# Kernel optimization log

Hardware: AMD Instinct MI355X
Metric: run time of the kernel (lower is better)

Reference implementation:

```python
import jax, jax.numpy as jnp
import numpy as np
import itertools

B, RES, RES_, STRIDE = 256, 14, 7, 2
N, N_ = RES * RES, RES_ * RES_
IN_DIM, OUT_DIM = 384, 512
H, KD, AR = 12, 32, 2
D = AR * KD            # 64, per-head value dim
DH = D * H             # 768
NH_KD = KD * H         # 384
KV_H = DH + NH_KD      # 1152
EPS = 1e-5


def _bias_idxs():
    # Replicates the relative-offset indexing from __init__.
    points = list(itertools.product(range(RES), range(RES)))
    points_ = list(itertools.product(range(RES_), range(RES_)))
    offsets, idxs = {}, []
    for p1 in points_:
        for p2 in points:
            off = (abs(p1[0] * STRIDE - p2[0]), abs(p1[1] * STRIDE - p2[1]))
            if off not in offsets:
                offsets[off] = len(offsets)
            idxs.append(offsets[off])
    return np.array(idxs, dtype=np.int32).reshape(N_, N), len(offsets)


def linear_bn(x, w, gamma, beta, mean, var):
    # Linear (no bias) followed by BatchNorm1d in inference form (fused affine).
    s = gamma / jnp.sqrt(var + EPS)
    return jnp.matmul(x, w.T) * s + (beta - mean * s)


def setup_inputs() -> dict:
    key = jax.random.key(0)
    ks = jax.random.split(key, 12)
    idxs_np, n_off = _bias_idxs()

    def bn_params(k, dim):
        k1, k2, k3, k4 = jax.random.split(k, 4)
        return (jax.random.normal(k1, (dim,)) * 0.1 + 1.0,   # gamma
                jax.random.normal(k2, (dim,)) * 0.1,          # beta
                jax.random.normal(k3, (dim,)) * 0.1,          # running_mean
                jax.random.uniform(k4, (dim,), minval=0.5, maxval=1.5))  # running_var

    kv_g, kv_b, kv_m, kv_v = bn_params(ks[1], KV_H)
    q_g, q_b, q_m, q_v = bn_params(ks[3], NH_KD)
    pr_g, pr_b, pr_m, pr_v = bn_params(ks[5], OUT_DIM)

    return {
        "x": jax.random.normal(ks[0], (B, N, IN_DIM), dtype=jnp.float32),
        "kv_w": jax.random.normal(ks[6], (KV_H, IN_DIM), dtype=jnp.float32) * (IN_DIM ** -0.5),
        "kv_g": kv_g, "kv_b": kv_b, "kv_m": kv_m, "kv_v": kv_v,
        "q_w": jax.random.normal(ks[7], (NH_KD, IN_DIM), dtype=jnp.float32) * (IN_DIM ** -0.5),
        "q_g": q_g, "q_b": q_b, "q_m": q_m, "q_v": q_v,
        "proj_w": jax.random.normal(ks[8], (OUT_DIM, DH), dtype=jnp.float32) * (DH ** -0.5),
        "proj_g": pr_g, "proj_b": pr_b, "proj_m": pr_m, "proj_v": pr_v,
        "attention_biases": jax.random.normal(ks[9], (H, n_off), dtype=jnp.float32) * 0.02,
        "bias_idxs": jnp.asarray(idxs_np),
    }


def reference(x, kv_w, kv_g, kv_b, kv_m, kv_v,
              q_w, q_g, q_b, q_m, q_v,
              proj_w, proj_g, proj_b, proj_m, proj_v,
              attention_biases, bias_idxs):
    Bsz = x.shape[0]
    scale = KD ** -0.5
    # kv projection: [B, N, H, KD+D] -> split into k, v
    kv = linear_bn(x, kv_w, kv_g, kv_b, kv_m, kv_v).reshape(Bsz, N, H, KD + D)
    k, v = kv[..., :KD], kv[..., KD:]
    # strided subsample of queries: [B, 14, 14, C] -> [B, 49, C]
    xs = x.reshape(Bsz, RES, RES, IN_DIM)[:, ::STRIDE, ::STRIDE].reshape(Bsz, N_, IN_DIM)
    q = linear_bn(xs, q_w, q_g, q_b, q_m, q_v).reshape(Bsz, N_, H, KD)
    # attention with gathered relative-position bias: bias [H, N_, N]
    bias = attention_biases[:, bias_idxs]
    attn = jnp.einsum('bqhd,bkhd->bhqk', q, k) * scale + bias
    attn = jax.nn.softmax(attn, axis=-1)
    out = jnp.einsum('bhqk,bkhd->bqhd', attn, v).reshape(Bsz, N_, DH)
    out = jax.nn.hard_swish(out)
    return linear_bn(out, proj_w, proj_g, proj_b, proj_m, proj_v)
```

## Files before the change

kernel.cpp:

```cpp
#include <hip/hip_runtime.h>
#include <hip/hip_bf16.h>
#include <math.h>

typedef unsigned short U16;
typedef unsigned int U32;
typedef __attribute__((ext_vector_type(8))) short bf8;
typedef __attribute__((ext_vector_type(4))) float f4;
typedef __attribute__((ext_vector_type(4))) unsigned short u16x4;

#define AS1 __attribute__((address_space(1)))
#define AS3 __attribute__((address_space(3)))

#define BSZ   256
#define NTOK  196
#define NQ    49
#define INDIM 384
#define OUTD  512
#define NH    12
#define DV    64
#define DHD   768
#define KVH   1152

#define FA0 0
#define FA1 8192
#define FB0 16384
#define FB1 20480
#define KL  0
#define QL  7168
#define VL  9216
#define PA  24576
#define FNK 12

__device__ inline U16 f2bf(float f){
    __hip_bfloat16 h = __float2bfloat16(f);
    return *(U16*)&h;
}
__device__ inline f4 f4zero(){ f4 z; z[0]=0.f; z[1]=0.f; z[2]=0.f; z[3]=0.f; return z; }

__global__ void k_cast8(const float* __restrict__ in, U16* __restrict__ out, int n8){
    int i = blockIdx.x*256 + threadIdx.x;
    if (i >= n8) return;
    const float* p = in + (size_t)i*8;
    U16 o[8];
#pragma unroll
    for (int j=0;j<8;++j) o[j] = f2bf(p[j]);
    *(bf8*)(out + (size_t)i*8) = *(const bf8*)o;
}

#define W1C (KVH*INDIM/8)
#define W2C (INDIM*INDIM/8)
#define W3C (OUTD*DHD/8)
__global__ void k_castw(const float* __restrict__ w1, const float* __restrict__ w2,
                        const float* __restrict__ w3, U16* __restrict__ o1,
                        U16* __restrict__ o2, U16* __restrict__ o3){
    int i = blockIdx.x*256 + threadIdx.x;
    const float* p; U16* o;
    if (i < W1C){ p = w1 + (size_t)i*8; o = o1 + (size_t)i*8; }
    else if (i < W1C+W2C){ int k=i-W1C; p = w2 + (size_t)k*8; o = o2 + (size_t)k*8; }
    else if (i < W1C+W2C+W3C){ int k=i-W1C-W2C; p = w3 + (size_t)k*8; o = o3 + (size_t)k*8; }
    else return;
    U16 t[8];
#pragma unroll
    for (int j=0;j<8;++j) t[j] = f2bf(p[j]);
    *(bf8*)o = *(const bf8*)t;
}

#define BIAS_N   (NH*NQ*NTOK)
#define BIAS_BLK ((BIAS_N+255)/256)
#define BN_N     (KVH+INDIM+OUTD)
#define BN_BLK   (BN_N/256)
__global__ void k_misc(const float* __restrict__ ab, const int* __restrict__ idxs, int n_off,
                       const float* __restrict__ g1, const float* __restrict__ b1,
                       const float* __restrict__ m1, const float* __restrict__ v1,
                       const float* __restrict__ g2, const float* __restrict__ b2,
                       const float* __restrict__ m2, const float* __restrict__ v2,
                       const float* __restrict__ g3, const float* __restrict__ b3,
                       const float* __restrict__ m3, const float* __restrict__ v3,
                       float* __restrict__ s1, float* __restrict__ bo1,
                       float* __restrict__ s2, float* __restrict__ bo2,
                       float* __restrict__ s3, float* __restrict__ bo3,
                       float* __restrict__ bias_out){
    int blk = blockIdx.x;
    int tid = threadIdx.x;
    if (blk < BIAS_BLK){
        int i = blk*256 + tid;
        if (i < BIAS_N){
            int h = i / (NQ*NTOK);
            int qk = i - h*(NQ*NTOK);
            bias_out[i] = ab[h*n_off + idxs[qk]];
        }
    } else {
        int i = (blk-BIAS_BLK)*256 + tid;
        const float *g,*b,*m,*v; float *so,*bo; int k;
        if (i < KVH){ g=g1;b=b1;m=m1;v=v1;so=s1;bo=bo1;k=i; }
        else if (i < KVH+INDIM){ g=g2;b=b2;m=m2;v=v2;so=s2;bo=bo2;k=i-KVH; }
        else { g=g3;b=b3;m=m3;v=v3;so=s3;bo=bo3;k=i-KVH-INDIM; }
        float s = g[k] / sqrtf(v[k] + 1e-5f);
        so[k] = s;
        bo[k] = b[k] - m[k]*s;
    }
}

__global__ __launch_bounds__(256,2) void k_fused(
    const U16* __restrict__ xbf, const U16* __restrict__ kvw, const U16* __restrict__ qw,
    const float* __restrict__ skv, const float* __restrict__ bkv,
    const float* __restrict__ sq,  const float* __restrict__ bq,
    const float* __restrict__ biasf, U16* __restrict__ aout)
{
    __shared__ U16 smem[32768];
    const int bh_hw = blockIdx.x;
    const int bh = (bh_hw & 7)*384 + (bh_hw >> 3);
    const int b  = bh / NH, h = bh - b*NH;
    const int tid = threadIdx.x, lane = tid & 63, w = tid >> 6;
    const int wm = w >> 1, wn = w & 1;
    const int l15 = lane & 15, oct = lane >> 4;

    U16* Ab[2] = { smem + FA0, smem + FA1 };
    U16* Bb[2] = { smem + FB0, smem + FB1 };

    const U16* abase = xbf + ((size_t)(b*NTOK + tid))*INDIM;
    const U16* bsrc[2];
    {
        int row = tid & 127;
#pragma unroll
        for (int c=0;c<2;++c){
            int ch = c*2 + (tid>>7);
            bsrc[c] = (row < 96) ? kvw + ((size_t)(h*96 + row))*INDIM + ch*8
                                 : qw  + ((size_t)(h*32 + (row-96)))*INDIM + ch*8;
        }
    }

    f4 acc[8][4];
#pragma unroll
    for (int i=0;i<8;++i)
#pragma unroll
        for (int j=0;j<4;++j) acc[i][j] = f4zero();

#pragma unroll
    for (int c=0;c<4;++c)
        __builtin_amdgcn_global_load_lds((const AS1 U32*)(abase + c*8),
            (AS3 U32*)(Ab[0] + (c*256+tid)*8), 16, 0, 0);
#pragma unroll
    for (int c=0;c<2;++c)
        __builtin_amdgcn_global_load_lds((const AS1 U32*)(bsrc[c]),
            (AS3 U32*)(Bb[0] + (c*256+tid)*8), 16, 0, 0);

#pragma unroll
    for (int kt=0; kt<FNK; ++kt){
        const int cur = kt & 1;
        if (kt+1 < FNK){
            const int kb = (kt+1)*32;
#pragma unroll
            for (int c=0;c<4;++c)
                __builtin_amdgcn_global_load_lds((const AS1 U32*)(abase + kb + c*8),
                    (AS3 U32*)(Ab[cur^1] + (c*256+tid)*8), 16, 0, 0);
#pragma unroll
            for (int c=0;c<2;++c)
                __builtin_amdgcn_global_load_lds((const AS1 U32*)(bsrc[c] + kb),
                    (AS3 U32*)(Bb[cur^1] + (c*256+tid)*8), 16, 0, 0);
            asm volatile("s_waitcnt vmcnt(6)" ::: "memory");
        } else {
            asm volatile("s_waitcnt vmcnt(0)" ::: "memory");
        }
        __builtin_amdgcn_sched_barrier(0);
        __builtin_amdgcn_s_barrier();
        __builtin_amdgcn_sched_barrier(0);

        bf8 af[8], bfr[4];
#pragma unroll
        for (int i=0;i<8;++i)
            af[i]  = *(const bf8*)(Ab[cur] + (oct*256 + wm*128 + i*16 + l15)*8);
#pragma unroll
        for (int j=0;j<4;++j)
            bfr[j] = *(const bf8*)(Bb[cur] + (oct*128 + wn*64 + j*16 + l15)*8);
        __builtin_amdgcn_s_setprio(1);
#pragma unroll
        for (int i=0;i<8;++i)
#pragma unroll
            for (int j=0;j<4;++j)
                acc[i][j] = __builtin_amdgcn_mfma_f32_16x16x32_bf16(af[i], bfr[j], acc[i][j], 0, 0, 0);
        __builtin_amdgcn_s_setprio(0);
        __builtin_amdgcn_sched_barrier(0);
        __builtin_amdgcn_s_barrier();
        __builtin_amdgcn_sched_barrier(0);
    }

#pragma unroll
    for (int j=0;j<4;++j){
        const int c = wn*64 + j*16 + l15;
        float sc, bi;
        if (c < 96){ sc = skv[h*96 + c]; bi = bkv[h*96 + c]; }
        else       { sc = sq[h*32 + (c-96)]; bi = bq[h*32 + (c-96)]; }
#pragma unroll
        for (int i=0;i<8;++i){
            if (wm == 1 && i >= 6) continue;
            const int n0 = wm*128 + i*16 + oct*4;
            if (c < 32){
#pragma unroll
                for (int r=0;r<4;++r)
                    smem[KL + ((c>>3)*224 + (n0+r))*8 + (c&7)] = f2bf(acc[i][j][r]*sc + bi);
            } else if (c < 96){
                const int dv = c - 32;
                u16x4 pk;
#pragma unroll
                for (int r=0;r<4;++r) pk[r] = f2bf(acc[i][j][r]*sc + bi);
                *(u16x4*)(smem + VL + ((n0>>3)*64 + dv)*8 + (oct&1)*4) = pk;
            } else {
                const int dq = c - 96;
#pragma unroll
                for (int r=0;r<4;++r){
                    const int n = n0 + r;
                    if (n < 196 && (n & 1) == 0){
                        const int dn = n / 28, nm = n - dn*28;
                        if (nm < 14){
                            const int qg2 = dn*7 + (nm >> 1);
                            smem[QL + ((dq>>3)*64 + qg2)*8 + (dq&7)] = f2bf(acc[i][j][r]*sc + bi);
                        }
                    }
                }
            }
        }
    }
    __syncthreads();

    const int qg = w*16 + l15;
    const bf8 qf = *(const bf8*)(smem + QL + (oct*64 + qg)*8);

    f4 sacc[14];
#pragma unroll
    for (int mt=0;mt<14;++mt) sacc[mt] = f4zero();
#pragma unroll
    for (int mt=0;mt<14;++mt){
        const bf8 kf = *(const bf8*)(smem + KL + (oct*224 + mt*16 + l15)*8);
        sacc[mt] = __builtin_amdgcn_mfma_f32_16x16x32_bf16(kf, qf, sacc[mt], 0, 0, 0);
    }
    __syncthreads();

    const float scale = 0.17677669529663689f;
    float mx = -1e30f;
#pragma unroll
    for (int mt=0;mt<14;++mt){
        const int n0 = mt*16 + oct*4;
        f4 bi4 = f4zero();
        if (qg < NQ && n0 < 196) bi4 = *(const f4*)(biasf + ((size_t)h*NQ + qg)*NTOK + n0);
#pragma unroll
        for (int r=0;r<4;++r){
            float s = (n0 + r < NTOK) ? sacc[mt][r]*scale + bi4[r] : -1e30f;
            sacc[mt][r] = s;
            mx = fmaxf(mx, s);
        }
    }
    mx = fmaxf(mx, __shfl_xor(mx, 16));
    mx = fmaxf(mx, __shfl_xor(mx, 32));

    float sum = 0.f;
#pragma unroll
    for (int mt=0;mt<14;++mt){
#pragma unroll
        for (int r=0;r<4;++r){
            float p = (mt*16 + oct*4 + r < NTOK) ? __expf(sacc[mt][r] - mx) : 0.f;
            sacc[mt][r] = p;
            sum += p;
        }
    }
    sum += __shfl_xor(sum, 16);
    sum += __shfl_xor(sum, 32);
    const float inv = 1.f / sum;

    const int prow = w*16 + l15;
    const int pbase = ((w < 2) ? PA : 0) + (prow & 31)*224;
    const int psw = prow & 3;
#pragma unroll
    for (int mt=0;mt<14;++mt){
        u16x4 pk;
#pragma unroll
        for (int r=0;r<4;++r) pk[r] = f2bf(sacc[mt][r]*inv);
        const int blk = (mt*2 + (oct>>1)) ^ psw;
        *(u16x4*)(smem + pbase + blk*8 + (oct&1)*4) = pk;
    }

    f4 pacc[4];
#pragma unroll
    for (int dt=0;dt<4;++dt) pacc[dt] = f4zero();
#pragma unroll
    for (int kt=0;kt<7;++kt){
        const bf8 pa = *(const bf8*)(smem + pbase + ((kt*4 + oct) ^ psw)*8);
#pragma unroll
        for (int dt=0;dt<4;++dt){
            const bf8 vf = *(const bf8*)(smem + VL + ((kt*4 + oct)*64 + dt*16 + l15)*8);
            pacc[dt] = __builtin_amdgcn_mfma_f32_16x16x32_bf16(pa, vf, pacc[dt], 0, 0, 0);
        }
    }

#pragma unroll
    for (int dt=0;dt<4;++dt){
#pragma unroll
        for (int r=0;r<4;++r){
            const int qo = w*16 + oct*4 + r;
            if (qo < NQ){
                const int d = dt*16 + l15;
                float v = pacc[dt][r];
                float t = fminf(fmaxf(v + 3.f, 0.f), 6.f);
                aout[((size_t)(b*NQ + qo))*DHD + h*DV + d] = f2bf(v * t * (1.f/6.f));
            }
        }
    }
}

__global__ __launch_bounds__(256,2) void k_proj(
    const U16* __restrict__ A, const U16* __restrict__ Bw,
    const float* __restrict__ s_arr, const float* __restrict__ b_arr,
    float* __restrict__ o32)
{
    __shared__ U16 smem[32768];
    U16* Ab[2] = { smem,          smem + 8192 };
    U16* Bb[2] = { smem + 16384,  smem + 24576 };
    const int l   = (blockIdx.x & 7)*49 + (blockIdx.x >> 3);
    const int gn0 = (l & 3) * 128;
    const int gm0 = (l >> 2) * 128;
    const int tid  = threadIdx.x;
    const int lane = tid & 63;
    const int w    = tid >> 6;
    const int wm   = w >> 1, wn = w & 1;
    const int l15  = lane & 15, oct = lane >> 4;

    f4 acc[4][4];
#pragma unroll
    for (int i=0;i<4;++i)
#pragma unroll
        for (int j=0;j<4;++j) acc[i][j] = f4zero();

    size_t aoff[4], boff[4];
#pragma unroll
    for (int c=0;c<4;++c){
        int slot = c*256 + tid;
        int row = slot & 127, ch = slot >> 7;
        aoff[c] = (size_t)(gm0 + row)*DHD + ch*8;
        boff[c] = (size_t)(gn0 + row)*DHD + ch*8;
    }

#pragma unroll
    for (int c=0;c<4;++c){
        __builtin_amdgcn_global_load_lds((const AS1 U32*)(A + aoff[c]),
            (AS3 U32*)(Ab[0] + (c*256+tid)*8), 16, 0, 0);
        __builtin_amdgcn_global_load_lds((const AS1 U32*)(Bw + boff[c]),
            (AS3 U32*)(Bb[0] + (c*256+tid)*8), 16, 0, 0);
    }

#pragma unroll
    for (int kt=0; kt<12; ++kt){
        const int cur = kt & 1;
        if (kt+1 < 12){
            const int kb = (kt+1)*64;
#pragma unroll
            for (int c=0;c<4;++c){
                __builtin_amdgcn_global_load_lds((const AS1 U32*)(A + aoff[c] + kb),
                    (AS3 U32*)(Ab[cur^1] + (c*256+tid)*8), 16, 0, 0);
                __builtin_amdgcn_global_load_lds((const AS1 U32*)(Bw + boff[c] + kb),
                    (AS3 U32*)(Bb[cur^1] + (c*256+tid)*8), 16, 0, 0);
            }
            asm volatile("s_waitcnt vmcnt(8)" ::: "memory");
        } else {
            asm volatile("s_waitcnt vmcnt(0)" ::: "memory");
        }
        __builtin_amdgcn_sched_barrier(0);
        __builtin_amdgcn_s_barrier();
        __builtin_amdgcn_sched_barrier(0);

#pragma unroll
        for (int kk=0;kk<2;++kk){
            bf8 af[4], bfr[4];
#pragma unroll
            for (int i=0;i<4;++i)
                af[i]  = *(const bf8*)(Ab[cur] + ((kk*4+oct)*128 + wm*64 + i*16 + l15)*8);
#pragma unroll
            for (int j=0;j<4;++j)
                bfr[j] = *(const bf8*)(Bb[cur] + ((kk*4+oct)*128 + wn*64 + j*16 + l15)*8);
            __builtin_amdgcn_s_setprio(1);
#pragma unroll
            for (int i=0;i<4;++i)
#pragma unroll
                for (int j=0;j<4;++j)
                    acc[i][j] = __builtin_amdgcn_mfma_f32_16x16x32_bf16(af[i], bfr[j], acc[i][j], 0, 0, 0);
            __builtin_amdgcn_s_setprio(0);
        }
        __builtin_amdgcn_sched_barrier(0);
        __builtin_amdgcn_s_barrier();
        __builtin_amdgcn_sched_barrier(0);
    }

#pragma unroll
    for (int j=0;j<4;++j){
        const int col = gn0 + wn*64 + j*16 + l15;
        const float sc = s_arr[col];
        const float bi = b_arr[col];
#pragma unroll
        for (int i=0;i<4;++i){
            const int row0 = gm0 + wm*64 + i*16 + oct*4;
#pragma unroll
            for (int r=0;r<4;++r)
                o32[(size_t)(row0+r)*OUTD + col] = acc[i][j][r]*sc + bi;
        }
    }
}

extern "C" void kernel_launch(void* const* d_in, const int* in_sizes, int n_in,
                              void* d_out, int out_size, void* d_ws, size_t ws_size,
                              hipStream_t stream)
{
    const float* x    = (const float*)d_in[0];
    const float* kv_w = (const float*)d_in[1];
    const float* kv_g = (const float*)d_in[2];
    const float* kv_b = (const float*)d_in[3];
    const float* kv_m = (const float*)d_in[4];
    const float* kv_v = (const float*)d_in[5];
    const float* q_w  = (const float*)d_in[6];
    const float* q_g  = (const float*)d_in[7];
    const float* q_b  = (const float*)d_in[8];
    const float* q_m  = (const float*)d_in[9];
    const float* q_v  = (const float*)d_in[10];
    const float* pr_w = (const float*)d_in[11];
    const float* pr_g = (const float*)d_in[12];
    const float* pr_b = (const float*)d_in[13];
    const float* pr_m = (const float*)d_in[14];
    const float* pr_v = (const float*)d_in[15];
    const float* ab   = (const float*)d_in[16];
    const int*  idxs  = (const int*)d_in[17];
    const int n_off = in_sizes[16] / NH;

    char* ws = (char*)d_ws;
    size_t off = 0;
    auto alloc = [&](size_t bytes)->char*{
        char* p = ws + off; off += (bytes + 255) & ~(size_t)255; return p;
    };
    U16*   x_bf   = (U16*)  alloc((size_t)BSZ*NTOK*INDIM*2);
    U16*   kvw_bf = (U16*)  alloc((size_t)KVH*INDIM*2);
    U16*   qw_bf  = (U16*)  alloc((size_t)INDIM*INDIM*2);
    U16*   prw_bf = (U16*)  alloc((size_t)OUTD*DHD*2);
    float* s_kv   = (float*)alloc(KVH*4);
    float* b_kv   = (float*)alloc(KVH*4);
    float* s_q    = (float*)alloc(INDIM*4);
    float* b_q    = (float*)alloc(INDIM*4);
    float* s_pr   = (float*)alloc(OUTD*4);
    float* b_pr   = (float*)alloc(OUTD*4);
    float* biasf  = (float*)alloc(((size_t)NH*NQ*NTOK + 256)*4);
    U16*   a_out  = (U16*)  alloc((size_t)BSZ*NQ*DHD*2);
    if (off > ws_size) return;

    {
        int n8 = BSZ*NTOK*INDIM/8;
        k_cast8<<<(n8+255)/256, 256, 0, stream>>>(x, x_bf, n8);
    }
    k_castw<<<(W1C+W2C+W3C+255)/256, 256, 0, stream>>>(kv_w, q_w, pr_w, kvw_bf, qw_bf, prw_bf);
    k_misc<<<BIAS_BLK+BN_BLK, 256, 0, stream>>>(
        ab, idxs, n_off,
        kv_g, kv_b, kv_m, kv_v, q_g, q_b, q_m, q_v, pr_g, pr_b, pr_m, pr_v,
        s_kv, b_kv, s_q, b_q, s_pr, b_pr, biasf);

    k_fused<<<BSZ*NH, 256, 0, stream>>>(x_bf, kvw_bf, qw_bf, s_kv, b_kv, s_q, b_q,
                                        biasf, a_out);

    k_proj<<<392, 256, 0, stream>>>(a_out, prw_bf, s_pr, b_pr, (float*)d_out);
}
```

Baseline: 216.0 us.

## Process two heads per block and move Q projection to a separate GEMM

The fused attention kernel now handles a pair of heads per 512-thread block, so each x tile loaded into LDS is reused across two heads' K/V projections. It uses a zero-padded 224-row x copy and a K step of 64. The Q projection, previously computed inside the fused kernel over all 196 tokens and then subsampled, now runs as a dedicated GEMM over only the 49 strided query rows, cutting wasted MFMA work. The cost is extra launches, a larger padded x buffer, a q_out round trip through global memory, and more LDS per block, which may reduce occupancy.

```diff
diff --git a/kernel.cpp b/kernel.cpp
--- a/kernel.cpp
+++ b/kernel.cpp
@@ -20,27 +20,45 @@
 #define DV    64
 #define DHD   768
 #define KVH   1152
-
-#define FA0 0
-#define FA1 8192
-#define FB0 16384
-#define FB1 20480
-#define KL  0
-#define QL  7168
-#define VL  9216
-#define PA  24576
-#define FNK 12
+#define NPADR 224
 
 __device__ inline U16 f2bf(float f){
     __hip_bfloat16 h = __float2bfloat16(f);
     return *(U16*)&h;
 }
 __device__ inline f4 f4zero(){ f4 z; z[0]=0.f; z[1]=0.f; z[2]=0.f; z[3]=0.f; return z; }
-
-__global__ void k_cast8(const float* __restrict__ in, U16* __restrict__ out, int n8){
+__device__ inline bf8 bf8zero(){ bf8 v;
+#pragma unroll
+    for (int j=0;j<8;++j) v[j]=0; return v; }
+
+__global__ void k_cast8p(const float* __restrict__ in, U16* __restrict__ out, int n8){
     int i = blockIdx.x*256 + threadIdx.x;
     if (i >= n8) return;
-    const float* p = in + (size_t)i*8;
+    int rall = i / 48;
+    int c8   = i - rall*48;
+    int b    = rall / NPADR;
+    int r    = rall - b*NPADR;
+    U16 o[8];
+    if (r < NTOK){
+        const float* p = in + ((size_t)(b*NTOK + r))*INDIM + c8*8;
+#pragma unroll
+        for (int j=0;j<8;++j) o[j] = f2bf(p[j]);
+    } else {
+#pragma unroll
+        for (int j=0;j<8;++j) o[j] = 0;
+    }
+    *(bf8*)(out + (size_t)i*8) = *(const bf8*)o;
+}
+
+__global__ void k_castxs(const float* __restrict__ x, U16* __restrict__ out, int n8){
+    int i = blockIdx.x*256 + threadIdx.x;
+    if (i >= n8) return;
+    int row = i / 48;
+    int c8  = i - row*48;
+    int b   = row / 49;
+    int q   = row - b*49;
+    int r_  = q / 7, c_ = q - r_*7;
+    const float* p = x + ((size_t)(b*NTOK + 28*r_ + 2*c_))*INDIM + c8*8;
     U16 o[8];
 #pragma unroll
     for (int j=0;j<8;++j) o[j] = f2bf(p[j]);
@@ -67,8 +85,7 @@
 
 #define BIAS_N   (NH*NQ*NTOK)
 #define BIAS_BLK ((BIAS_N+255)/256)
-#define BN_N     (KVH+INDIM+OUTD)
-#define BN_BLK   (BN_N/256)
+#define BN_BLK   ((KVH+INDIM+OUTD)/256)
 __global__ void k_misc(const float* __restrict__ ab, const int* __restrict__ idxs, int n_off,
                        const float* __restrict__ g1, const float* __restrict__ b1,
                        const float* __restrict__ m1, const float* __restrict__ v1,
@@ -101,64 +118,71 @@
     }
 }
 
-__global__ __launch_bounds__(256,2) void k_fused(
-    const U16* __restrict__ xbf, const U16* __restrict__ kvw, const U16* __restrict__ qw,
+__global__ __launch_bounds__(512,2) void k_fused(
+    const U16* __restrict__ xbf, const U16* __restrict__ kvw, const U16* __restrict__ qo_,
     const float* __restrict__ skv, const float* __restrict__ bkv,
-    const float* __restrict__ sq,  const float* __restrict__ bq,
     const float* __restrict__ biasf, U16* __restrict__ aout)
 {
-    __shared__ U16 smem[32768];
-    const int bh_hw = blockIdx.x;
-    const int bh = (bh_hw & 7)*384 + (bh_hw >> 3);
-    const int b  = bh / NH, h = bh - b*NH;
+    __shared__ U16 smem[57344];
+    const int hw = blockIdx.x;
+    const int pair = (hw & 7)*192 + (hw >> 3);
+    const int b = pair / 6, hp = pair - b*6;
     const int tid = threadIdx.x, lane = tid & 63, w = tid >> 6;
-    const int wm = w >> 1, wn = w & 1;
+    const int wm = w & 1, wc = w >> 1;
     const int l15 = lane & 15, oct = lane >> 4;
 
-    U16* Ab[2] = { smem + FA0, smem + FA1 };
-    U16* Bb[2] = { smem + FB0, smem + FB1 };
-
-    const U16* abase = xbf + ((size_t)(b*NTOK + tid))*INDIM;
-    const U16* bsrc[2];
-    {
-        int row = tid & 127;
-#pragma unroll
-        for (int c=0;c<2;++c){
-            int ch = c*2 + (tid>>7);
-            bsrc[c] = (row < 96) ? kvw + ((size_t)(h*96 + row))*INDIM + ch*8
-                                 : qw  + ((size_t)(h*32 + (row-96)))*INDIM + ch*8;
-        }
-    }
-
-    f4 acc[8][4];
-#pragma unroll
-    for (int i=0;i<8;++i)
-#pragma unroll
-        for (int j=0;j<4;++j) acc[i][j] = f4zero();
-
-#pragma unroll
-    for (int c=0;c<4;++c)
-        __builtin_amdgcn_global_load_lds((const AS1 U32*)(abase + c*8),
-            (AS3 U32*)(Ab[0] + (c*256+tid)*8), 16, 0, 0);
-#pragma unroll
-    for (int c=0;c<2;++c)
-        __builtin_amdgcn_global_load_lds((const AS1 U32*)(bsrc[c]),
-            (AS3 U32*)(Bb[0] + (c*256+tid)*8), 16, 0, 0);
-
-#pragma unroll
-    for (int kt=0; kt<FNK; ++kt){
+    U16* Ab[2] = { smem + 0,     smem + 14336 };
+    U16* Bb[2] = { smem + 28672, smem + 40960 };
+
+    U32 aoff[4];
+#pragma unroll
+    for (int c=0;c<3;++c){
+        int s = c*512 + tid;
+        int ach = s / NPADR, ar = s - ach*NPADR;
+        aoff[c] = (U32)(b*NPADR + ar)*INDIM + ach*8;
+    }
+    if (tid >= 256){
+        int s = 1280 + tid;
+        int ach = s / NPADR, ar = s - ach*NPADR;
+        aoff[3] = (U32)(b*NPADR + ar)*INDIM + ach*8;
+    }
+    U32 boff[3];
+#pragma unroll
+    for (int c=0;c<3;++c){
+        int s = c*512 + tid;
+        int bch = s / 192, br = s - bch*192;
+        boff[c] = (U32)(hp*192 + br)*INDIM + bch*8;
+    }
+
+    f4 acc[7][3];
+#pragma unroll
+    for (int i=0;i<7;++i)
+#pragma unroll
+        for (int j=0;j<3;++j) acc[i][j] = f4zero();
+
+#define STAGE(buf, kb) do{ \
+    _Pragma("unroll") \
+    for (int c=0;c<3;++c) \
+        __builtin_amdgcn_global_load_lds((const AS1 U32*)(xbf + aoff[c] + (kb)), \
+            (AS3 U32*)(Ab[buf] + (c*512+tid)*8), 16, 0, 0); \
+    if (tid >= 256) \
+        __builtin_amdgcn_global_load_lds((const AS1 U32*)(xbf + aoff[3] + (kb)), \
+            (AS3 U32*)(Ab[buf] + (1280+tid)*8), 16, 0, 0); \
+    _Pragma("unroll") \
+    for (int c=0;c<3;++c) \
+        __builtin_amdgcn_global_load_lds((const AS1 U32*)(kvw + boff[c] + (kb)), \
+            (AS3 U32*)(Bb[buf] + (c*512+tid)*8), 16, 0, 0); \
+}while(0)
+
+    STAGE(0, 0);
+
+#pragma unroll
+    for (int kt=0; kt<6; ++kt){
         const int cur = kt & 1;
-        if (kt+1 < FNK){
-            const int kb = (kt+1)*32;
-#pragma unroll
-            for (int c=0;c<4;++c)
-                __builtin_amdgcn_global_load_lds((const AS1 U32*)(abase + kb + c*8),
-                    (AS3 U32*)(Ab[cur^1] + (c*256+tid)*8), 16, 0, 0);
-#pragma unroll
-            for (int c=0;c<2;++c)
-                __builtin_amdgcn_global_load_lds((const AS1 U32*)(bsrc[c] + kb),
-                    (AS3 U32*)(Bb[cur^1] + (c*256+tid)*8), 16, 0, 0);
-            asm volatile("s_waitcnt vmcnt(6)" ::: "memory");
+        if (kt < 5){
+            STAGE(cur^1, (kt+1)*64);
+            if (w < 4) asm volatile("s_waitcnt vmcnt(6)" ::: "memory");
+            else       asm volatile("s_waitcnt vmcnt(7)" ::: "memory");
         } else {
             asm volatile("s_waitcnt vmcnt(0)" ::: "memory");
         }
@@ -166,75 +190,72 @@
         __builtin_amdgcn_s_barrier();
         __builtin_amdgcn_sched_barrier(0);
 
-        bf8 af[8], bfr[4];
-#pragma unroll
-        for (int i=0;i<8;++i)
-            af[i]  = *(const bf8*)(Ab[cur] + (oct*256 + wm*128 + i*16 + l15)*8);
-#pragma unroll
-        for (int j=0;j<4;++j)
-            bfr[j] = *(const bf8*)(Bb[cur] + (oct*128 + wn*64 + j*16 + l15)*8);
-        __builtin_amdgcn_s_setprio(1);
-#pragma unroll
-        for (int i=0;i<8;++i)
-#pragma unroll
-            for (int j=0;j<4;++j)
-                acc[i][j] = __builtin_amdgcn_mfma_f32_16x16x32_bf16(af[i], bfr[j], acc[i][j], 0, 0, 0);
-        __builtin_amdgcn_s_setprio(0);
+#pragma unroll
+        for (int kk=0;kk<2;++kk){
+            bf8 af[7], bfr[3];
+#pragma unroll
+            for (int i=0;i<7;++i)
+                af[i]  = *(const bf8*)(Ab[cur] + ((kk*4+oct)*NPADR + wm*112 + i*16 + l15)*8);
+#pragma unroll
+            for (int j=0;j<3;++j)
+                bfr[j] = *(const bf8*)(Bb[cur] + ((kk*4+oct)*192 + wc*48 + j*16 + l15)*8);
+            __builtin_amdgcn_s_setprio(1);
+#pragma unroll
+            for (int i=0;i<7;++i)
+#pragma unroll
+                for (int j=0;j<3;++j)
+                    acc[i][j] = __builtin_amdgcn_mfma_f32_16x16x32_bf16(af[i], bfr[j], acc[i][j], 0, 0, 0);
+            __builtin_amdgcn_s_setprio(0);
+        }
         __builtin_amdgcn_sched_barrier(0);
         __builtin_amdgcn_s_barrier();
         __builtin_amdgcn_sched_barrier(0);
     }
-
-#pragma unroll
-    for (int j=0;j<4;++j){
-        const int c = wn*64 + j*16 + l15;
-        float sc, bi;
-        if (c < 96){ sc = skv[h*96 + c]; bi = bkv[h*96 + c]; }
-        else       { sc = sq[h*32 + (c-96)]; bi = bq[h*32 + (c-96)]; }
-#pragma unroll
-        for (int i=0;i<8;++i){
-            if (wm == 1 && i >= 6) continue;
-            const int n0 = wm*128 + i*16 + oct*4;
-            if (c < 32){
+#undef STAGE
+
+    const int hT = wc >> 1;
+    const int hG = hp*2 + hT;
+    U16* KLt = smem + hT*28672;
+    U16* VLt = KLt + 7168;
+#pragma unroll
+    for (int j=0;j<3;++j){
+        const int cc = (wc&1)*48 + j*16 + l15;
+        const float sc = skv[hG*96 + cc];
+        const float bi = bkv[hG*96 + cc];
+#pragma unroll
+        for (int i=0;i<7;++i){
+            const int n0 = wm*112 + i*16 + oct*4;
+            if (cc < 32){
 #pragma unroll
                 for (int r=0;r<4;++r)
-                    smem[KL + ((c>>3)*224 + (n0+r))*8 + (c&7)] = f2bf(acc[i][j][r]*sc + bi);
-            } else if (c < 96){
-                const int dv = c - 32;
+                    KLt[((cc>>3)*NPADR + n0 + r)*8 + (cc&7)] = f2bf(acc[i][j][r]*sc + bi);
+            } else {
+                const int dv = cc - 32;
                 u16x4 pk;
 #pragma unroll
                 for (int r=0;r<4;++r) pk[r] = f2bf(acc[i][j][r]*sc + bi);
-                *(u16x4*)(smem + VL + ((n0>>3)*64 + dv)*8 + (oct&1)*4) = pk;
-            } else {
-                const int dq = c - 96;
-#pragma unroll
-                for (int r=0;r<4;++r){
-                    const int n = n0 + r;
-                    if (n < 196 && (n & 1) == 0){
-                        const int dn = n / 28, nm = n - dn*28;
-                        if (nm < 14){
-                            const int qg2 = dn*7 + (nm >> 1);
-                            smem[QL + ((dq>>3)*64 + qg2)*8 + (dq&7)] = f2bf(acc[i][j][r]*sc + bi);
-                        }
-                    }
-                }
+                *(u16x4*)(VLt + ((n0>>3)*64 + dv)*8 + (oct&1)*4) = pk;
             }
         }
     }
     __syncthreads();
 
-    const int qg = w*16 + l15;
-    const bf8 qf = *(const bf8*)(smem + QL + (oct*64 + qg)*8);
+    const int t = w >> 2;
+    const int h = hp*2 + t;
+    U16* KLa = smem + t*28672;
+    U16* VLa = KLa + 7168;
+    const int qg = (w&3)*16 + l15;
+    bf8 qf = bf8zero();
+    if (qg < NQ) qf = *(const bf8*)(qo_ + ((size_t)(b*NQ + qg))*INDIM + h*32 + oct*8);
 
     f4 sacc[14];
 #pragma unroll
     for (int mt=0;mt<14;++mt) sacc[mt] = f4zero();
 #pragma unroll
     for (int mt=0;mt<14;++mt){
-        const bf8 kf = *(const bf8*)(smem + KL + (oct*224 + mt*16 + l15)*8);
+        const bf8 kf = *(const bf8*)(KLa + (oct*NPADR + mt*16 + l15)*8);
         sacc[mt] = __builtin_amdgcn_mfma_f32_16x16x32_bf16(kf, qf, sacc[mt], 0, 0, 0);
     }
-    __syncthreads();
 
     const float scale = 0.17677669529663689f;
     float mx = -1e30f;
@@ -242,7 +263,7 @@
     for (int mt=0;mt<14;++mt){
         const int n0 = mt*16 + oct*4;
         f4 bi4 = f4zero();
-        if (qg < NQ && n0 < 196) bi4 = *(const f4*)(biasf + ((size_t)h*NQ + qg)*NTOK + n0);
+        if (qg < NQ && n0 < NTOK) bi4 = *(const f4*)(biasf + ((size_t)h*NQ + qg)*NTOK + n0);
 #pragma unroll
         for (int r=0;r<4;++r){
             float s = (n0 + r < NTOK) ? sacc[mt][r]*scale + bi4[r] : -1e30f;
@@ -267,8 +288,10 @@
     sum += __shfl_xor(sum, 32);
     const float inv = 1.f / sum;
 
-    const int prow = w*16 + l15;
-    const int pbase = ((w < 2) ? PA : 0) + (prow & 31)*224;
+    __syncthreads();
+
+    const int prow = (w&3)*16 + l15;
+    const int pbase = t*28672 + ((prow < 32) ? (21504 + prow*NPADR) : ((prow-32)*NPADR));
     const int psw = prow & 3;
 #pragma unroll
     for (int mt=0;mt<14;++mt){
@@ -287,7 +310,7 @@
         const bf8 pa = *(const bf8*)(smem + pbase + ((kt*4 + oct) ^ psw)*8);
 #pragma unroll
         for (int dt=0;dt<4;++dt){
-            const bf8 vf = *(const bf8*)(smem + VL + ((kt*4 + oct)*64 + dt*16 + l15)*8);
+            const bf8 vf = *(const bf8*)(VLa + ((kt*4 + oct)*64 + dt*16 + l15)*8);
             pacc[dt] = __builtin_amdgcn_mfma_f32_16x16x32_bf16(pa, vf, pacc[dt], 0, 0, 0);
         }
     }
@@ -296,13 +319,109 @@
     for (int dt=0;dt<4;++dt){
 #pragma unroll
         for (int r=0;r<4;++r){
-            const int qo = w*16 + oct*4 + r;
-            if (qo < NQ){
+            const int qo2 = (w&3)*16 + oct*4 + r;
+            if (qo2 < NQ){
                 const int d = dt*16 + l15;
                 float v = pacc[dt][r];
-                float t = fminf(fmaxf(v + 3.f, 0.f), 6.f);
-                aout[((size_t)(b*NQ + qo))*DHD + h*DV + d] = f2bf(v * t * (1.f/6.f));
+                float tt = fminf(fmaxf(v + 3.f, 0.f), 6.f);
+                aout[((size_t)(b*NQ + qo2))*DHD + h*DV + d] = f2bf(v * tt * (1.f/6.f));
             }
+        }
+    }
+}
+
+__global__ __launch_bounds__(256,2) void k_qgemm(
+    const U16* __restrict__ A, const U16* __restrict__ Bw,
+    const float* __restrict__ s_arr, const float* __restrict__ b_arr,
+    U16* __restrict__ o16)
+{
+    __shared__ U16 smem[32768];
+    U16* Ab[2] = { smem,          smem + 8192 };
+    U16* Bb[2] = { smem + 16384,  smem + 24576 };
+    const int gn0 = blockIdx.x * 128;
+    const int gm0 = blockIdx.y * 128;
+    const int tid  = threadIdx.x;
+    const int lane = tid & 63;
+    const int w    = tid >> 6;
+    const int wm   = w >> 1, wn = w & 1;
+    const int l15  = lane & 15, oct = lane >> 4;
+
+    f4 acc[4][4];
+#pragma unroll
+    for (int i=0;i<4;++i)
+#pragma unroll
+        for (int j=0;j<4;++j) acc[i][j] = f4zero();
+
+    size_t aoff[4], boff[4];
+#pragma unroll
+    for (int c=0;c<4;++c){
+        int slot = c*256 + tid;
+        int row = slot & 127, ch = slot >> 7;
+        aoff[c] = (size_t)(gm0 + row)*INDIM + ch*8;
+        boff[c] = (size_t)(gn0 + row)*INDIM + ch*8;
+    }
+
+#pragma unroll
+    for (int c=0;c<4;++c){
+        __builtin_amdgcn_global_load_lds((const AS1 U32*)(A + aoff[c]),
+            (AS3 U32*)(Ab[0] + (c*256+tid)*8), 16, 0, 0);
+        __builtin_amdgcn_global_load_lds((const AS1 U32*)(Bw + boff[c]),
+            (AS3 U32*)(Bb[0] + (c*256+tid)*8), 16, 0, 0);
+    }
+
+#pragma unroll
+    for (int kt=0; kt<6; ++kt){
+        const int cur = kt & 1;
+        if (kt+1 < 6){
+            const int kb = (kt+1)*64;
+#pragma unroll
+            for (int c=0;c<4;++c){
+                __builtin_amdgcn_global_load_lds((const AS1 U32*)(A + aoff[c] + kb),
+                    (AS3 U32*)(Ab[cur^1] + (c*256+tid)*8), 16, 0, 0);
+                __builtin_amdgcn_global_load_lds((const AS1 U32*)(Bw + boff[c] + kb),
+                    (AS3 U32*)(Bb[cur^1] + (c*256+tid)*8), 16, 0, 0);
+            }
+            asm volatile("s_waitcnt vmcnt(8)" ::: "memory");
+        } else {
+            asm volatile("s_waitcnt vmcnt(0)" ::: "memory");
+        }
+        __builtin_amdgcn_sched_barrier(0);
+        __builtin_amdgcn_s_barrier();
+        __builtin_amdgcn_sched_barrier(0);
+
+#pragma unroll
+        for (int kk=0;kk<2;++kk){
+            bf8 af[4], bfr[4];
+#pragma unroll
+            for (int i=0;i<4;++i)
+                af[i]  = *(const bf8*)(Ab[cur] + ((kk*4+oct)*128 + wm*64 + i*16 + l15)*8);
+#pragma unroll
+            for (int j=0;j<4;++j)
+                bfr[j] = *(const bf8*)(Bb[cur] + ((kk*4+oct)*128 + wn*64 + j*16 + l15)*8);
+            __builtin_amdgcn_s_setprio(1);
+#pragma unroll
+            for (int i=0;i<4;++i)
+#pragma unroll
+                for (int j=0;j<4;++j)
+                    acc[i][j] = __builtin_amdgcn_mfma_f32_16x16x32_bf16(af[i], bfr[j], acc[i][j], 0, 0, 0);
+            __builtin_amdgcn_s_setprio(0);
+        }
+        __builtin_amdgcn_sched_barrier(0);
+        __builtin_amdgcn_s_barrier();
+        __builtin_amdgcn_sched_barrier(0);
+    }
+
+#pragma unroll
+    for (int j=0;j<4;++j){
+        const int col = gn0 + wn*64 + j*16 + l15;
+        const float sc = s_arr[col];
+        const float bi = b_arr[col];
+#pragma unroll
+        for (int i=0;i<4;++i){
+            const int row0 = gm0 + wm*64 + i*16 + oct*4;
+#pragma unroll
+            for (int r=0;r<4;++r)
+                o16[(size_t)(row0+r)*INDIM + col] = f2bf(acc[i][j][r]*sc + bi);
         }
     }
 }
@@ -433,7 +552,8 @@
     auto alloc = [&](size_t bytes)->char*{
         char* p = ws + off; off += (bytes + 255) & ~(size_t)255; return p;
     };
-    U16*   x_bf   = (U16*)  alloc((size_t)BSZ*NTOK*INDIM*2);
+    U16*   x_bf   = (U16*)  alloc((size_t)BSZ*NPADR*INDIM*2);
+    U16*   xs_bf  = (U16*)  alloc((size_t)BSZ*NQ*INDIM*2);
     U16*   kvw_bf = (U16*)  alloc((size_t)KVH*INDIM*2);
     U16*   qw_bf  = (U16*)  alloc((size_t)INDIM*INDIM*2);
     U16*   prw_bf = (U16*)  alloc((size_t)OUTD*DHD*2);
@@ -444,12 +564,17 @@
     float* s_pr   = (float*)alloc(OUTD*4);
     float* b_pr   = (float*)alloc(OUTD*4);
     float* biasf  = (float*)alloc(((size_t)NH*NQ*NTOK + 256)*4);
+    U16*   q_out  = (U16*)  alloc((size_t)BSZ*NQ*INDIM*2);
     U16*   a_out  = (U16*)  alloc((size_t)BSZ*NQ*DHD*2);
     if (off > ws_size) return;
 
     {
-        int n8 = BSZ*NTOK*INDIM/8;
-        k_cast8<<<(n8+255)/256, 256, 0, stream>>>(x, x_bf, n8);
+        int n8 = BSZ*NPADR*INDIM/8;
+        k_cast8p<<<(n8+255)/256, 256, 0, stream>>>(x, x_bf, n8);
+    }
+    {
+        int n8 = BSZ*NQ*INDIM/8;
+        k_castxs<<<(n8+255)/256, 256, 0, stream>>>(x, xs_bf, n8);
     }
     k_castw<<<(W1C+W2C+W3C+255)/256, 256, 0, stream>>>(kv_w, q_w, pr_w, kvw_bf, qw_bf, prw_bf);
     k_misc<<<BIAS_BLK+BN_BLK, 256, 0, stream>>>(
@@ -457,8 +582,10 @@
         kv_g, kv_b, kv_m, kv_v, q_g, q_b, q_m, q_v, pr_g, pr_b, pr_m, pr_v,
         s_kv, b_kv, s_q, b_q, s_pr, b_pr, biasf);
 
-    k_fused<<<BSZ*NH, 256, 0, stream>>>(x_bf, kvw_bf, qw_bf, s_kv, b_kv, s_q, b_q,
-                                        biasf, a_out);
-
+    {
+        dim3 g(INDIM/128, BSZ*NQ/128);
+        k_qgemm<<<g, 256, 0, stream>>>(xs_bf, qw_bf, s_q, b_q, q_out);
+    }
+    k_fused<<<BSZ*NH/2, 512, 0, stream>>>(x_bf, kvw_bf, q_out, s_kv, b_kv, biasf, a_out);
     k_proj<<<392, 256, 0, stream>>>(a_out, prw_bf, s_pr, b_pr, (float*)d_out);
 }
```

Result: faster. 200.4 us (-7.2%).
